# Kernel optimization log

Measured on AMD Instinct MI355X. Metric: run time of the kernel, lower is better.

Reference implementation:

```python
import jax, jax.numpy as jnp
import numpy as np

N_HASHES = 8
BUCKET_SIZE = 64


def setup_inputs() -> dict:
    key = jax.random.key(0)
    k1, k2, k3 = jax.random.split(key, 3)
    B, S, D = 16, 4096, 64
    n_buckets = S // BUCKET_SIZE  # 64
    qk = jax.random.normal(k1, (B, S, D), jnp.float32)
    v = jax.random.normal(k2, (B, S, D), jnp.float32)
    # random rotations (shared across batch, per hash round): (1, D, n_hashes, n_buckets//2)
    rotations = jax.random.normal(k3, (1, D, N_HASHES, n_buckets // 2), jnp.float32)
    return {"qk": qk, "v": v, "rotations": rotations}


def _look_one_back(x):
    # concat each chunk with the previous chunk (wrap-around), along the within-chunk axis
    x_extra = jnp.roll(x, 1, axis=1)
    return jnp.concatenate([x, x_extra], axis=2)


def _lsh_attention(qk, v, rotations):
    B, S, D = qk.shape
    n_buckets = S // BUCKET_SIZE

    # ---- hash_vectors ----
    rot = jnp.broadcast_to(rotations, (B, D, N_HASHES, n_buckets // 2))
    rotated = jnp.einsum('btf,bfhi->bhti', qk, rot)           # [B, H, S, nb/2]
    rotated = jnp.concatenate([rotated, -rotated], axis=-1)    # [B, H, S, nb]
    buckets = jnp.argmax(rotated, axis=-1)                     # [B, H, S]
    offsets = (jnp.arange(N_HASHES) * n_buckets).reshape(1, -1, 1)
    buckets = (buckets + offsets).reshape(B, -1)               # [B, H*S]

    # ---- sort by (bucket, position) ----
    total = N_HASHES * S
    ticker = jnp.arange(total)
    buckets_and_t = S * buckets + (ticker % S)[None, :]        # unique keys
    sticker = jnp.argsort(buckets_and_t, axis=-1)              # sort order
    undo_sort = jnp.argsort(sticker, axis=-1)

    st = sticker % S                                           # original positions
    sqk = jnp.take_along_axis(qk, st[..., None], axis=1)       # [B, H*S, D]
    sv = jnp.take_along_axis(v, st[..., None], axis=1)

    chunk_size = N_HASHES * n_buckets                          # number of chunks
    bq_t = st.reshape(B, chunk_size, -1)                       # [B, C, bs]
    bqk = sqk.reshape(B, chunk_size, -1, D)                    # [B, C, bs, D]
    bv = sv.reshape(B, chunk_size, -1, D)

    bq = bqk
    bk = bqk / jnp.clip(jnp.linalg.norm(bqk, axis=-1, keepdims=True), 1e-12)

    bk = _look_one_back(bk)                                    # [B, C, 2*bs, D]
    bv = _look_one_back(bv)
    bkv_t = _look_one_back(bq_t)                               # [B, C, 2*bs]

    dots = jnp.einsum('bhie,bhje->bhij', bq, bk) * (D ** -0.5)  # [B, C, bs, 2*bs]

    # mask self-attention (token attending to itself)
    self_mask = bq_t[:, :, :, None] == bkv_t[:, :, None, :]
    dots = jnp.where(self_mask, jnp.float32(-1e5), dots)

    lse = jax.nn.logsumexp(dots, axis=-1, keepdims=True)
    probs = jnp.exp(dots - lse)
    bo = jnp.einsum('buij,buje->buie', probs, bv)              # [B, C, bs, D]

    so = bo.reshape(B, -1, D)                                  # [B, H*S, D]
    slogits = lse.reshape(B, -1)                               # [B, H*S]

    # unsort back to original order
    o = jnp.take_along_axis(so, undo_sort[..., None], axis=1)
    logits = jnp.take_along_axis(slogits, undo_sort, axis=1)

    o = o.reshape(B, N_HASHES, S, D)
    logits = logits.reshape(B, N_HASHES, S, 1)

    # combine hash rounds by normalized logsumexp weights
    w = jnp.exp(logits - jax.nn.logsumexp(logits, axis=1, keepdims=True))
    out = jnp.sum(o * w, axis=1)                               # [B, S, D]
    return out, buckets


def reference(qk, v, rotations):
    return _lsh_attention(qk, v, rotations)
```

## Files before the change

### kernel.cpp

```cpp
#include <hip/hip_runtime.h>
#include <hip/hip_bf16.h>
#include <math.h>

#define B 16
#define S 4096
#define D 64
#define NH 8
#define NBUCK 64
#define CHUNKS 512
#define BS 64

#define GAP_MFMA 0.12f

typedef __attribute__((ext_vector_type(8))) short s8_t;
typedef __attribute__((ext_vector_type(4))) float f4_t;
typedef __attribute__((ext_vector_type(2))) unsigned int u32x2;

__device__ inline unsigned short bf16_rne(float x) {
    unsigned int u = __float_as_uint(x);
    u += 0x7fffu + ((u >> 16) & 1u);
    return (unsigned short)(u >> 16);
}
__device__ inline unsigned int pack_bf16_pair(float x0, float x1) {
    return (unsigned int)bf16_rne(x0) | ((unsigned int)bf16_rne(x1) << 16);
}
__device__ inline void split_bf16(float x, unsigned short& h, unsigned short& l) {
    h = bf16_rne(x);
    float hf = __uint_as_float(((unsigned int)h) << 16);
    l = bf16_rne(x - hf);
}
__device__ inline unsigned int pack_trunc(float x0, float x1) {
    return __builtin_amdgcn_perm(__float_as_uint(x1), __float_as_uint(x0),
                                 0x07060302u);
}
__device__ inline unsigned short bf16_trunc(float x) {
    return (unsigned short)(__float_as_uint(x) >> 16);
}

#define BAR_LGKM() do {                                          \
    asm volatile("s_waitcnt lgkmcnt(0)" ::: "memory");           \
    __builtin_amdgcn_s_barrier();                                \
    asm volatile("" ::: "memory");                               \
} while (0)

template<int OFF>
__device__ inline u32x2 tr_read(unsigned int vaddr) {
    u32x2 d;
    asm volatile("ds_read_b64_tr_b16 %0, %1 offset:%c2"
                 : "=v"(d) : "v"(vaddr), "i"(OFF));
    return d;
}

#define HA_OFF 0
#define HQH_OFF 36864
#define HQL_OFF 55296
#define HLDS_TOT 73728
#define HSTR 144

__global__ __launch_bounds__(256, 2) void hash_kernel(
    const float* __restrict__ qk, const float* __restrict__ rot,
    float* __restrict__ out_buckets, int* __restrict__ bucket_ws,
    unsigned char* __restrict__ flag_ws)
{
    __shared__ char lds[HLDS_TOT];
    int tid = threadIdx.x;
    int wg = blockIdx.x;
    int orig = ((wg & 7) << 6) + (wg >> 3);
    int b    = orig >> 5;
    int tile = orig & 31;
    int token0 = tile * 128;

    {
        char* arow = lds + HA_OFF + tid * HSTR;
        #pragma unroll 4
        for (int f = 0; f < 64; f += 2) {
            float r0 = rot[(size_t)f * 256 + tid];
            float r1 = rot[(size_t)(f + 1) * 256 + tid];
            *(unsigned int*)(arow + f * 2) = pack_bf16_pair(r0, r1);
        }
    }
    {
        int wv0   = tid >> 6;
        int lane0 = tid & 63;
        int s_ = lane0 & 3;
        int rowA = wv0 * 32 + (lane0 >> 2);
        int rowB = rowA + 16;
        const float4* qA = (const float4*)(qk + ((size_t)b * S + token0 + rowA) * D);
        const float4* qB = (const float4*)(qk + ((size_t)b * S + token0 + rowB) * D);
        float4 a4[4], b4[4];
        #pragma unroll
        for (int n = 0; n < 4; ++n) { a4[n] = qA[n * 4 + s_]; b4[n] = qB[n * 4 + s_]; }

        char* qhA = lds + HQH_OFF + rowA * HSTR;
        char* qlA = lds + HQL_OFF + rowA * HSTR;
        char* qhB = lds + HQH_OFF + rowB * HSTR;
        char* qlB = lds + HQL_OFF + rowB * HSTR;
        #pragma unroll
        for (int n = 0; n < 4; ++n) {
            float fa[4] = {a4[n].x, a4[n].y, a4[n].z, a4[n].w};
            float fb[4] = {b4[n].x, b4[n].y, b4[n].z, b4[n].w};
            unsigned short h[4], l[4];
            #pragma unroll
            for (int e = 0; e < 4; ++e) split_bf16(fa[e], h[e], l[e]);
            *(uint2*)(qhA + n * 32 + s_ * 8) =
                make_uint2((unsigned)h[0] | ((unsigned)h[1] << 16),
                           (unsigned)h[2] | ((unsigned)h[3] << 16));
            *(uint2*)(qlA + n * 32 + s_ * 8) =
                make_uint2((unsigned)l[0] | ((unsigned)l[1] << 16),
                           (unsigned)l[2] | ((unsigned)l[3] << 16));
            #pragma unroll
            for (int e = 0; e < 4; ++e) split_bf16(fb[e], h[e], l[e]);
            *(uint2*)(qhB + n * 32 + s_ * 8) =
                make_uint2((unsigned)h[0] | ((unsigned)h[1] << 16),
                           (unsigned)h[2] | ((unsigned)h[3] << 16));
            *(uint2*)(qlB + n * 32 + s_ * 8) =
                make_uint2((unsigned)l[0] | ((unsigned)l[1] << 16),
                           (unsigned)l[2] | ((unsigned)l[3] << 16));
        }
    }
    __syncthreads();

    int wv   = tid >> 6;
    int lane = tid & 63;
    int quad = lane >> 4;
    int cc   = lane & 15;

    for (int nt = 0; nt < 2; ++nt) {
        int ntg = wv * 2 + nt;
        const char* qrh = lds + HQH_OFF + (ntg * 16 + cc) * HSTR + quad * 16;
        const char* qrl = lds + HQL_OFF + (ntg * 16 + cc) * HSTR + quad * 16;
        s8_t bh0 = *(const s8_t*)(qrh);
        s8_t bh1 = *(const s8_t*)(qrh + 64);
        s8_t bl0 = *(const s8_t*)(qrl);
        s8_t bl1 = *(const s8_t*)(qrl + 64);

        float v1 = -3e38f, v2 = -3e38f;
        int i1 = 0;

        for (int mt = 0; mt < 16; ++mt) {
            const char* arow = lds + HA_OFF + (mt * 16 + cc) * HSTR + quad * 16;
            s8_t a0 = *(const s8_t*)(arow);
            s8_t a1 = *(const s8_t*)(arow + 64);
            f4_t acc = (f4_t){0.f, 0.f, 0.f, 0.f};
            acc = __builtin_amdgcn_mfma_f32_16x16x32_bf16(a0, bh0, acc, 0, 0, 0);
            acc = __builtin_amdgcn_mfma_f32_16x16x32_bf16(a1, bh1, acc, 0, 0, 0);
            acc = __builtin_amdgcn_mfma_f32_16x16x32_bf16(a0, bl0, acc, 0, 0, 0);
            acc = __builtin_amdgcn_mfma_f32_16x16x32_bf16(a1, bl1, acc, 0, 0, 0);

            if ((mt & 1) == 0) { v1 = -3e38f; v2 = -3e38f; i1 = 0; }
            int ibase = ((mt & 1) << 4) + (quad << 2);
            #pragma unroll
            for (int r = 0; r < 4; ++r) {
                float vp = acc[r];
                int ip = ibase + r;
                v2 = fmaxf(v2, fminf(vp, v1));
                if (vp > v1) { v1 = vp; i1 = ip; }
                float vn = -vp;
                v2 = fmaxf(v2, fminf(vn, v1));
                if (vn > v1) { v1 = vn; i1 = ip + 32; }
            }

            if (mt & 1) {
                #pragma unroll
                for (int off = 16; off <= 32; off <<= 1) {
                    float ov1 = __shfl_xor(v1, off, 64);
                    float ov2 = __shfl_xor(v2, off, 64);
                    int   oi1 = __shfl_xor(i1, off, 64);
                    float nv2 = fmaxf(fmaxf(v2, ov2), fminf(v1, ov1));
                    if (ov1 > v1) { v1 = ov1; i1 = oi1; }
                    v2 = nv2;
                }
                if (quad == 0) {
                    int h = mt >> 1;
                    int tok = token0 + ntg * 16 + cc;
                    size_t idx = (size_t)(b * NH + h) * S + tok;
                    bucket_ws[idx] = i1;
                    out_buckets[idx] = (float)(i1 + h * NBUCK);
                    flag_ws[idx] = (v1 - v2 < GAP_MFMA) ? 1 : 0;
                }
            }
        }
    }
}

__global__ __launch_bounds__(256) void hash_fixup_kernel(
    const float* __restrict__ qk, const float* __restrict__ rot,
    const unsigned char* __restrict__ flag_ws,
    float* __restrict__ out_buckets, int* __restrict__ bucket_ws)
{
    __shared__ int list[2048];
    __shared__ int cnt;
    int tid = threadIdx.x;
    if (tid == 0) cnt = 0;
    __syncthreads();

    int base = blockIdx.x * 2048;
    for (int i = tid; i < 2048; i += 256) {
        if (flag_ws[base + i]) {
            int slot = atomicAdd(&cnt, 1);
            list[slot] = base + i;
        }
    }
    __syncthreads();
    int n = cnt;

    for (int j = tid; j < n; j += 256) {
        int gid = list[j];
        int bh = gid >> 12, t = gid & (S - 1);
        int b = bh >> 3, h = bh & 7;
        const float* row = qk + ((size_t)b * S + t) * D;

        double acc[32];
        #pragma unroll
        for (int i = 0; i < 32; ++i) acc[i] = 0.0;
        for (int f = 0; f < 64; ++f) {
            double x = (double)row[f];
            const float* rr = rot + f * (NH * 32) + h * 32;
            #pragma unroll
            for (int i = 0; i < 32; ++i)
                acc[i] = __fma_rn(x, (double)rr[i], acc[i]);
        }
        double best = acc[0]; int bi = 0;
        double worst = acc[0]; int wi = 0;
        #pragma unroll
        for (int i = 1; i < 32; ++i) {
            if (acc[i] > best)  { best = acc[i]; bi = i; }
            if (acc[i] < worst) { worst = acc[i]; wi = i; }
        }
        int bucket = (-worst > best) ? (32 + wi) : bi;
        bucket_ws[gid] = bucket;
        out_buckets[gid] = (float)(bucket + h * NBUCK);
    }
}

__global__ __launch_bounds__(512) void sort_kernel(
    const int* __restrict__ bucket_ws, int* __restrict__ st_ws)
{
    __shared__ int sb[S];
    __shared__ int hist[8][64];
    __shared__ int bpref[64];
    __shared__ int woff[8][64];

    int tid  = threadIdx.x;
    int wv   = tid >> 6;
    int lane = tid & 63;
    int base = blockIdx.x * S;

    hist[wv][lane] = 0;
    __syncthreads();

    int qbase = wv * 512;
    #pragma unroll
    for (int i = 0; i < 8; ++i) {
        int t = qbase + i * 64 + lane;
        int v = bucket_ws[base + t];
        sb[t] = v;
        atomicAdd(&hist[wv][v], 1);
    }
    __syncthreads();

    if (wv == 0) {
        int total = 0;
        #pragma unroll
        for (int w = 0; w < 8; ++w) total += hist[w][lane];
        int x = total;
        #pragma unroll
        for (int off = 1; off < 64; off <<= 1) {
            int y = __shfl_up(x, off, 64);
            if (lane >= off) x += y;
        }
        bpref[lane] = x - total;
    }
    __syncthreads();
    {
        int o = bpref[lane];
        for (int w2 = 0; w2 < 8; ++w2) {
            if (w2 < wv) o += hist[w2][lane];
        }
        woff[wv][lane] = o;
    }
    __syncthreads();

    for (int g = 0; g < 8; ++g) {
        int t = qbase + g * 64 + lane;
        int v = sb[t];

        unsigned long long m = ~0ULL;
        #pragma unroll
        for (int bit = 0; bit < 6; ++bit) {
            unsigned long long bm = __ballot((v >> bit) & 1);
            m &= ((v >> bit) & 1) ? bm : ~bm;
        }
        unsigned long long below = (lane == 63) ? ~0ULL >> 1
                                 : ((1ULL << lane) - 1ULL);
        int rank = __popcll(m & below);
        int cnt  = __popcll(m);

        int pos = woff[wv][v] + rank;
        st_ws[base + pos] = t;

        if ((m & below) == 0ULL)
            woff[wv][v] += cnt;
    }
}

#define OFF_VT 18432
#define OFF_NRM 35840
#define OFF_TKX 36352
#define OFF_PINV 36864
#define LDS_TOT 37120
#define KSTRB 144
#define PSTRB 272

template<int KC>
__device__ inline void pv_step(const char* lds, unsigned vaddr,
                               int wv, int cc, int quad, f4_t* oaccT)
{
    s8_t pb = *(const s8_t*)(lds + (wv * 16 + cc) * PSTRB + KC * 64 + quad * 16);
    u32x2 t00 = tr_read<KC * 4352 +    0>(vaddr);
    u32x2 t01 = tr_read<KC * 4352 +  544>(vaddr);
    u32x2 t10 = tr_read<KC * 4352 + 1088>(vaddr);
    u32x2 t11 = tr_read<KC * 4352 + 1632>(vaddr);
    u32x2 t20 = tr_read<KC * 4352 + 2176>(vaddr);
    u32x2 t21 = tr_read<KC * 4352 + 2720>(vaddr);
    u32x2 t30 = tr_read<KC * 4352 + 3264>(vaddr);
    u32x2 t31 = tr_read<KC * 4352 + 3808>(vaddr);
    asm volatile("s_waitcnt lgkmcnt(0)" ::: "memory");
    __builtin_amdgcn_sched_barrier(0);
    union { u32x2 d[2]; s8_t s; } u0, u1, u2, u3;
    u0.d[0] = t00; u0.d[1] = t01;
    u1.d[0] = t10; u1.d[1] = t11;
    u2.d[0] = t20; u2.d[1] = t21;
    u3.d[0] = t30; u3.d[1] = t31;
    oaccT[0] = __builtin_amdgcn_mfma_f32_16x16x32_bf16(u0.s, pb, oaccT[0], 0, 0, 0);
    oaccT[1] = __builtin_amdgcn_mfma_f32_16x16x32_bf16(u1.s, pb, oaccT[1], 0, 0, 0);
    oaccT[2] = __builtin_amdgcn_mfma_f32_16x16x32_bf16(u2.s, pb, oaccT[2], 0, 0, 0);
    oaccT[3] = __builtin_amdgcn_mfma_f32_16x16x32_bf16(u3.s, pb, oaccT[3], 0, 0, 0);
}

__global__ __launch_bounds__(256, 4) void attn_kernel(
    const float* __restrict__ qk, const float* __restrict__ v,
    const int* __restrict__ st_ws,
    __hip_bfloat16* __restrict__ o_ws, float* __restrict__ logits_ws)
{
    __shared__ char lds[LDS_TOT];
    float* nrm_s  = (float*)(lds + OFF_NRM);
    int*   tkx    = (int*)(lds + OFF_TKX);
    float* pinv_s = (float*)(lds + OFF_PINV);

    int tid = threadIdx.x;
    int wg = blockIdx.x;
    int orig = ((wg & 7) << 10) + (wg >> 3);
    int c = orig & (CHUNKS - 1);
    int b = orig >> 9;
    int h = c >> 6;
    int sbase = b * (NH * S);
    int cprev = (c + CHUNKS - 1) & (CHUNKS - 1);

    int wv   = tid >> 6;
    int lane = tid & 63;
    int quad = lane >> 4;
    int cc   = lane & 15;
    int s_   = lane & 3;

    int rowA = wv * 32 + (lane >> 2);
    int rowB = rowA + 16;
    int chK  = (wv < 2) ? c : cprev;
    int tokKA = st_ws[sbase + chK * BS + (rowA & 63)];
    int tokKB = st_ws[sbase + chK * BS + (rowB & 63)];
    const float4* kpA = (const float4*)(qk + ((size_t)b * S + tokKA) * D);
    const float4* kpB = (const float4*)(qk + ((size_t)b * S + tokKB) * D);
    float4 kA4[4], kB4[4];
    #pragma unroll
    for (int n = 0; n < 4; ++n) { kA4[n] = kpA[n * 4 + s_]; kB4[n] = kpB[n * 4 + s_]; }

    int prA = wv * 32 + (lane >> 2);
    int prB = prA + 16;
    int ciA = ((prA & 3) << 4) | (prA >> 3);
    int ciB = ((prB & 3) << 4) | (prB >> 3);
    int chVA = (prA & 4) ? cprev : c;
    int chVB = (prB & 4) ? cprev : c;
    int tokVA = st_ws[sbase + chVA * BS + ciA];
    int tokVB = st_ws[sbase + chVB * BS + ciB];
    const float4* vpA = (const float4*)(v + ((size_t)b * S + tokVA) * D);
    const float4* vpB = (const float4*)(v + ((size_t)b * S + tokVB) * D);
    float4 vA4[4], vB4[4];
    #pragma unroll
    for (int n = 0; n < 4; ++n) { vA4[n] = vpA[n * 4 + s_]; vB4[n] = vpB[n * 4 + s_]; }

    {
        float ssA = 0.f, ssB = 0.f;
        #pragma unroll
        for (int n = 0; n < 4; ++n) {
            ssA += kA4[n].x*kA4[n].x + kA4[n].y*kA4[n].y
                 + kA4[n].z*kA4[n].z + kA4[n].w*kA4[n].w;
            ssB += kB4[n].x*kB4[n].x + kB4[n].y*kB4[n].y
                 + kB4[n].z*kB4[n].z + kB4[n].w*kB4[n].w;
        }
        ssA += __shfl_xor(ssA, 1, 64); ssA += __shfl_xor(ssA, 2, 64);
        ssB += __shfl_xor(ssB, 1, 64); ssB += __shfl_xor(ssB, 2, 64);
        if (s_ == 0) {
            nrm_s[rowA] = 1.0f / fmaxf(sqrtf(ssA), 1e-12f);
            nrm_s[rowB] = 1.0f / fmaxf(sqrtf(ssB), 1e-12f);
            tkx[rowA] = tokKA;
            tkx[rowB] = tokKB;
        }
        #pragma unroll
        for (int n = 0; n < 4; ++n) {
            *(uint2*)(lds + rowA * KSTRB + n * 32 + s_ * 8) =
                make_uint2(pack_trunc(kA4[n].x, kA4[n].y),
                           pack_trunc(kA4[n].z, kA4[n].w));
            *(uint2*)(lds + rowB * KSTRB + n * 32 + s_ * 8) =
                make_uint2(pack_trunc(kB4[n].x, kB4[n].y),
                           pack_trunc(kB4[n].z, kB4[n].w));
        }
    }
    BAR_LGKM();

    int qrow = wv * 16 + cc;
    f4_t acc[8];
    #pragma unroll
    for (int t = 0; t < 8; ++t) acc[t] = (f4_t){0.f,0.f,0.f,0.f};

    __builtin_amdgcn_s_setprio(1);
    #pragma unroll
    for (int kc = 0; kc < 2; ++kc) {
        int aoff = kc * 64 + quad * 16;
        s8_t av = *(const s8_t*)(lds + qrow * KSTRB + aoff);
        #pragma unroll
        for (int t = 0; t < 8; ++t) {
            s8_t bv = *(const s8_t*)(lds + (t * 16 + cc) * KSTRB + aoff);
            acc[t] = __builtin_amdgcn_mfma_f32_16x16x32_bf16(av, bv, acc[t], 0, 0, 0);
        }
    }
    __builtin_amdgcn_s_setprio(0);

    {
        int kcA = prA >> 5, qA = (prA >> 3) & 3, rA = (prA >> 2) & 1, jA = prA & 3;
        int kcB = prB >> 5, qB = (prB >> 3) & 3, rB = (prB >> 2) & 1, jB = prB & 3;
        #pragma unroll
        for (int n = 0; n < 4; ++n) {
            *(uint2*)(lds + OFF_VT + (kcA * 8 + n * 2 + rA) * 544
                      + qA * 128 + jA * 32 + s_ * 8) =
                make_uint2(pack_trunc(vA4[n].x, vA4[n].y),
                           pack_trunc(vA4[n].z, vA4[n].w));
            *(uint2*)(lds + OFF_VT + (kcB * 8 + n * 2 + rB) * 544
                      + qB * 128 + jB * 32 + s_ * 8) =
                make_uint2(pack_trunc(vB4[n].x, vB4[n].y),
                           pack_trunc(vB4[n].z, vB4[n].w));
        }
    }

    float invsc[8];
    #pragma unroll
    for (int t = 0; t < 8; ++t)
        invsc[t] = nrm_s[t * 16 + cc] * 0.18033688f;

    #pragma unroll
    for (int t = 0; t < 8; ++t) {
        #pragma unroll
        for (int g = 0; g < 4; ++g)
            acc[t][g] = acc[t][g] * invsc[t];
        if (t == wv) {
            #pragma unroll
            for (int g = 0; g < 4; ++g)
                if (cc == quad * 4 + g) acc[t][g] = -3e5f;
        }
    }

    float mx[4];
    #pragma unroll
    for (int g = 0; g < 4; ++g) {
        float m = acc[0][g];
        #pragma unroll
        for (int t = 1; t < 8; ++t) m = fmaxf(m, acc[t][g]);
        mx[g] = m;
    }
    #pragma unroll
    for (int msk = 1; msk <= 8; msk <<= 1)
        #pragma unroll
        for (int g = 0; g < 4; ++g) mx[g] = fmaxf(mx[g], __shfl_xor(mx[g], msk, 64));

    float sm[4] = {0.f, 0.f, 0.f, 0.f};
    #pragma unroll
    for (int t = 0; t < 8; ++t)
        #pragma unroll
        for (int g = 0; g < 4; ++g) {
            float p = __builtin_amdgcn_exp2f(acc[t][g] - mx[g]);
            acc[t][g] = p;
            sm[g] += p;
        }
    #pragma unroll
    for (int msk = 1; msk <= 8; msk <<= 1)
        #pragma unroll
        for (int g = 0; g < 4; ++g) sm[g] += __shfl_xor(sm[g], msk, 64);

    int tqi[4];
    #pragma unroll
    for (int g = 0; g < 4; ++g) tqi[g] = tkx[wv * 16 + quad * 4 + g];

    if (cc == 0) {
        #pragma unroll
        for (int g = 0; g < 4; ++g) {
            int q = wv * 16 + quad * 4 + g;
            pinv_s[q] = 1.0f / sm[g];
            logits_ws[sbase + h * S + tqi[g]] =
                0.69314718f * (mx[g] + __log2f(sm[g]));
        }
    }

    BAR_LGKM();
    #pragma unroll
    for (int g = 0; g < 4; ++g) {
        int q = wv * 16 + quad * 4 + g;
        uint4 w;
        w.x = pack_trunc(acc[0][g], acc[1][g]);
        w.y = pack_trunc(acc[2][g], acc[3][g]);
        w.z = pack_trunc(acc[4][g], acc[5][g]);
        w.w = pack_trunc(acc[6][g], acc[7][g]);
        *(uint4*)(lds + q * PSTRB + cc * 16) = w;
    }

    f4_t oaccT[4];
    #pragma unroll
    for (int n = 0; n < 4; ++n) oaccT[n] = (f4_t){0.f,0.f,0.f,0.f};

    unsigned vaddr = (unsigned)(unsigned long long)(lds + OFF_VT)
                   + (unsigned)lane * 8u;

    __builtin_amdgcn_s_setprio(1);
    pv_step<0>(lds, vaddr, wv, cc, quad, oaccT);
    pv_step<1>(lds, vaddr, wv, cc, quad, oaccT);
    pv_step<2>(lds, vaddr, wv, cc, quad, oaccT);
    pv_step<3>(lds, vaddr, wv, cc, quad, oaccT);
    __builtin_amdgcn_s_setprio(0);

    {
        int q = wv * 16 + cc;
        int tok = tkx[q];
        float pq = pinv_s[q];
        __hip_bfloat16* op = o_ws + ((size_t)(sbase + h * S + tok)) * D + quad * 4;
        #pragma unroll
        for (int n = 0; n < 4; ++n) {
            uint2 pk2;
            pk2.x = pack_trunc(oaccT[n][0] * pq, oaccT[n][1] * pq);
            pk2.y = pack_trunc(oaccT[n][2] * pq, oaccT[n][3] * pq);
            *(uint2*)(op + n * 16) = pk2;
        }
    }
}

__global__ __launch_bounds__(256) void combine_kernel(
    const __hip_bfloat16* __restrict__ o_ws, const float* __restrict__ logits_ws,
    float* __restrict__ out)
{
    int gid = blockIdx.x * 256 + threadIdx.x;
    int token = gid >> 3;
    int d8 = gid & 7;
    int b = token >> 12;
    int t = token & (S - 1);
    int base = b * (NH * S) + t;

    float l[8];
    #pragma unroll
    for (int hh = 0; hh < 8; ++hh) l[hh] = logits_ws[base + hh * S];
    float m = l[0];
    #pragma unroll
    for (int hh = 1; hh < 8; ++hh) m = fmaxf(m, l[hh]);
    float w[8]; float ssum = 0.f;
    #pragma unroll
    for (int hh = 0; hh < 8; ++hh) { w[hh] = __expf(l[hh] - m); ssum += w[hh]; }
    float inv = 1.0f / ssum;

    float accv[8] = {0,0,0,0,0,0,0,0};
    #pragma unroll
    for (int hh = 0; hh < 8; ++hh) {
        uint4 pk = *(const uint4*)(o_ws + (size_t)(base + hh * S) * D + d8 * 8);
        float wh = w[hh] * inv;
        unsigned int ws_[4] = {pk.x, pk.y, pk.z, pk.w};
        #pragma unroll
        for (int e = 0; e < 4; ++e) {
            float lo = __uint_as_float(ws_[e] << 16);
            float hi = __uint_as_float(ws_[e] & 0xffff0000u);
            accv[2*e]   += wh * lo;
            accv[2*e+1] += wh * hi;
        }
    }
    float4* op = (float4*)(out + (size_t)token * D + d8 * 8);
    op[0] = make_float4(accv[0], accv[1], accv[2], accv[3]);
    op[1] = make_float4(accv[4], accv[5], accv[6], accv[7]);
}

extern "C" void kernel_launch(void* const* d_in, const int* in_sizes, int n_in,
                              void* d_out, int out_size, void* d_ws, size_t ws_size,
                              hipStream_t stream) {
    const float* qk  = (const float*)d_in[0];
    const float* v   = (const float*)d_in[1];
    const float* rot = (const float*)d_in[2];

    float* out         = (float*)d_out;
    float* out_buckets = out + (size_t)B * S * D;

    int*   bucket_ws = (int*)d_ws;
    int*   st_ws     = bucket_ws + (size_t)B * NH * S;
    float* logits_ws = (float*)(st_ws + (size_t)B * NH * S);
    __hip_bfloat16* o_ws = (__hip_bfloat16*)(logits_ws + (size_t)B * NH * S);
    unsigned char* flag_ws = (unsigned char*)(o_ws + (size_t)B * NH * S * D);

    hash_kernel<<<B * 32, 256, 0, stream>>>(qk, rot, out_buckets, bucket_ws,
                                            flag_ws);
    hash_fixup_kernel<<<(B * NH * S) / 2048, 256, 0, stream>>>(
        qk, rot, flag_ws, out_buckets, bucket_ws);
    sort_kernel<<<B * NH, 512, 0, stream>>>(bucket_ws, st_ws);
    attn_kernel<<<B * CHUNKS, 256, 0, stream>>>(qk, v, st_ws, o_ws, logits_ws);
    combine_kernel<<<(B * S * 8) / 256, 256, 0, stream>>>(o_ws, logits_ws, out);
}
```

Measured before the change: 194.8 us.

## Precompute bf16 rotations, widen sort/fixup parallelism, transpose logits layout

Adds a prep kernel that converts the rotation matrix to a bf16 row-major buffer once, so each hash workgroup copies it with wide vector loads instead of strided float loads. The fixup kernel now uses more, smaller blocks, and the sort kernel uses 1024 threads per block with 16 wave histograms. Logits are stored token-major so the combine kernel can read them with two float4 loads. Several divisions and sqrt calls become hardware rcp/rsq approximations, and the scale factor is folded into the stored norm. The changes add one extra kernel launch and trade slightly lower precision in the reciprocals for fewer instructions.

Result: slower. 200.2 us (+2.8%).

```diff
diff --git a/kernel.cpp b/kernel.cpp
--- a/kernel.cpp
+++ b/kernel.cpp
@@ -51,6 +51,20 @@
     return d;
 }
 
+__global__ __launch_bounds__(256) void prep_kernel(
+    const float* __restrict__ rot, unsigned short* __restrict__ rt)
+{
+    int tid = threadIdx.x;
+    int m = blockIdx.x * 16 + (tid >> 4);
+    int fq = tid & 15;
+    float r0 = rot[(size_t)(fq * 4 + 0) * 256 + m];
+    float r1 = rot[(size_t)(fq * 4 + 1) * 256 + m];
+    float r2 = rot[(size_t)(fq * 4 + 2) * 256 + m];
+    float r3 = rot[(size_t)(fq * 4 + 3) * 256 + m];
+    *(uint2*)(rt + m * 64 + fq * 4) =
+        make_uint2(pack_bf16_pair(r0, r1), pack_bf16_pair(r2, r3));
+}
+
 #define HA_OFF 0
 #define HQH_OFF 36864
 #define HQL_OFF 55296
@@ -58,7 +72,7 @@
 #define HSTR 144
 
 __global__ __launch_bounds__(256, 2) void hash_kernel(
-    const float* __restrict__ qk, const float* __restrict__ rot,
+    const float* __restrict__ qk, const unsigned short* __restrict__ rt,
     float* __restrict__ out_buckets, int* __restrict__ bucket_ws,
     unsigned char* __restrict__ flag_ws)
 {
@@ -71,12 +85,12 @@
     int token0 = tile * 128;
 
     {
-        char* arow = lds + HA_OFF + tid * HSTR;
-        #pragma unroll 4
-        for (int f = 0; f < 64; f += 2) {
-            float r0 = rot[(size_t)f * 256 + tid];
-            float r1 = rot[(size_t)(f + 1) * 256 + tid];
-            *(unsigned int*)(arow + f * 2) = pack_bf16_pair(r0, r1);
+        int row = tid >> 3, seg = tid & 7;
+        #pragma unroll
+        for (int p = 0; p < 8; ++p) {
+            int m = p * 32 + row;
+            uint4 vv = *(const uint4*)(rt + m * 64 + seg * 8);
+            *(uint4*)(lds + HA_OFF + m * HSTR + seg * 16) = vv;
         }
     }
     {
@@ -188,14 +202,14 @@
     const unsigned char* __restrict__ flag_ws,
     float* __restrict__ out_buckets, int* __restrict__ bucket_ws)
 {
-    __shared__ int list[2048];
+    __shared__ int list[512];
     __shared__ int cnt;
     int tid = threadIdx.x;
     if (tid == 0) cnt = 0;
     __syncthreads();
 
-    int base = blockIdx.x * 2048;
-    for (int i = tid; i < 2048; i += 256) {
+    int base = blockIdx.x * 512;
+    for (int i = tid; i < 512; i += 256) {
         if (flag_ws[base + i]) {
             int slot = atomicAdd(&cnt, 1);
             list[slot] = base + i;
@@ -233,13 +247,13 @@
     }
 }
 
-__global__ __launch_bounds__(512) void sort_kernel(
+__global__ __launch_bounds__(1024) void sort_kernel(
     const int* __restrict__ bucket_ws, int* __restrict__ st_ws)
 {
     __shared__ int sb[S];
-    __shared__ int hist[8][64];
+    __shared__ int hist[16][64];
     __shared__ int bpref[64];
-    __shared__ int woff[8][64];
+    __shared__ int woff[16][64];
 
     int tid  = threadIdx.x;
     int wv   = tid >> 6;
@@ -249,9 +263,9 @@
     hist[wv][lane] = 0;
     __syncthreads();
 
-    int qbase = wv * 512;
-    #pragma unroll
-    for (int i = 0; i < 8; ++i) {
+    int qbase = wv * 256;
+    #pragma unroll
+    for (int i = 0; i < 4; ++i) {
         int t = qbase + i * 64 + lane;
         int v = bucket_ws[base + t];
         sb[t] = v;
@@ -262,7 +276,7 @@
     if (wv == 0) {
         int total = 0;
         #pragma unroll
-        for (int w = 0; w < 8; ++w) total += hist[w][lane];
+        for (int w = 0; w < 16; ++w) total += hist[w][lane];
         int x = total;
         #pragma unroll
         for (int off = 1; off < 64; off <<= 1) {
@@ -274,14 +288,15 @@
     __syncthreads();
     {
         int o = bpref[lane];
-        for (int w2 = 0; w2 < 8; ++w2) {
+        #pragma unroll
+        for (int w2 = 0; w2 < 16; ++w2) {
             if (w2 < wv) o += hist[w2][lane];
         }
         woff[wv][lane] = o;
     }
     __syncthreads();
 
-    for (int g = 0; g < 8; ++g) {
+    for (int g = 0; g < 4; ++g) {
         int t = qbase + g * 64 + lane;
         int v = sb[t];
 
@@ -400,8 +415,8 @@
         ssA += __shfl_xor(ssA, 1, 64); ssA += __shfl_xor(ssA, 2, 64);
         ssB += __shfl_xor(ssB, 1, 64); ssB += __shfl_xor(ssB, 2, 64);
         if (s_ == 0) {
-            nrm_s[rowA] = 1.0f / fmaxf(sqrtf(ssA), 1e-12f);
-            nrm_s[rowB] = 1.0f / fmaxf(sqrtf(ssB), 1e-12f);
+            nrm_s[rowA] = __builtin_amdgcn_rsqf(fmaxf(ssA, 1e-24f)) * 0.18033688f;
+            nrm_s[rowB] = __builtin_amdgcn_rsqf(fmaxf(ssB, 1e-24f)) * 0.18033688f;
             tkx[rowA] = tokKA;
             tkx[rowB] = tokKB;
         }
@@ -454,7 +469,7 @@
     float invsc[8];
     #pragma unroll
     for (int t = 0; t < 8; ++t)
-        invsc[t] = nrm_s[t * 16 + cc] * 0.18033688f;
+        invsc[t] = nrm_s[t * 16 + cc];
 
     #pragma unroll
     for (int t = 0; t < 8; ++t) {
@@ -495,16 +510,13 @@
         #pragma unroll
         for (int g = 0; g < 4; ++g) sm[g] += __shfl_xor(sm[g], msk, 64);
 
-    int tqi[4];
-    #pragma unroll
-    for (int g = 0; g < 4; ++g) tqi[g] = tkx[wv * 16 + quad * 4 + g];
-
     if (cc == 0) {
         #pragma unroll
         for (int g = 0; g < 4; ++g) {
             int q = wv * 16 + quad * 4 + g;
-            pinv_s[q] = 1.0f / sm[g];
-            logits_ws[sbase + h * S + tqi[g]] =
+            int tq = tkx[q];
+            pinv_s[q] = __builtin_amdgcn_rcpf(sm[g]);
+            logits_ws[((size_t)b * S + tq) * NH + h] =
                 0.69314718f * (mx[g] + __log2f(sm[g]));
         }
     }
@@ -561,16 +573,16 @@
     int t = token & (S - 1);
     int base = b * (NH * S) + t;
 
-    float l[8];
-    #pragma unroll
-    for (int hh = 0; hh < 8; ++hh) l[hh] = logits_ws[base + hh * S];
+    const float4* lp = (const float4*)(logits_ws + (size_t)token * NH);
+    float4 la = lp[0], lb = lp[1];
+    float l[8] = {la.x, la.y, la.z, la.w, lb.x, lb.y, lb.z, lb.w};
     float m = l[0];
     #pragma unroll
     for (int hh = 1; hh < 8; ++hh) m = fmaxf(m, l[hh]);
     float w[8]; float ssum = 0.f;
     #pragma unroll
     for (int hh = 0; hh < 8; ++hh) { w[hh] = __expf(l[hh] - m); ssum += w[hh]; }
-    float inv = 1.0f / ssum;
+    float inv = __builtin_amdgcn_rcpf(ssum);
 
     float accv[8] = {0,0,0,0,0,0,0,0};
     #pragma unroll
@@ -606,12 +618,14 @@
     float* logits_ws = (float*)(st_ws + (size_t)B * NH * S);
     __hip_bfloat16* o_ws = (__hip_bfloat16*)(logits_ws + (size_t)B * NH * S);
     unsigned char* flag_ws = (unsigned char*)(o_ws + (size_t)B * NH * S * D);
-
-    hash_kernel<<<B * 32, 256, 0, stream>>>(qk, rot, out_buckets, bucket_ws,
+    unsigned short* rt_ws = (unsigned short*)(flag_ws + (size_t)B * NH * S);
+
+    prep_kernel<<<16, 256, 0, stream>>>(rot, rt_ws);
+    hash_kernel<<<B * 32, 256, 0, stream>>>(qk, rt_ws, out_buckets, bucket_ws,
                                             flag_ws);
-    hash_fixup_kernel<<<(B * NH * S) / 2048, 256, 0, stream>>>(
+    hash_fixup_kernel<<<(B * NH * S) / 512, 256, 0, stream>>>(
         qk, rot, flag_ws, out_buckets, bucket_ws);
-    sort_kernel<<<B * NH, 512, 0, stream>>>(bucket_ws, st_ws);
+    sort_kernel<<<B * NH, 1024, 0, stream>>>(bucket_ws, st_ws);
     attn_kernel<<<B * CHUNKS, 256, 0, stream>>>(qk, v, st_ws, o_ws, logits_ws);
     combine_kernel<<<(B * S * 8) / 256, 256, 0, stream>>>(o_ws, logits_ws, out);
 }
```
